# Performance work log

Measured on AMD Instinct MI355X. Metric: run time of the kernel, lower is better.

Reference implementation:

```python
import jax, jax.numpy as jnp
import numpy as np

N = 262144
BN_EPS = 1e-5


def gcn_conv(x, edge_index, edge_weight, W, b):
    """PyG GCNConv: symmetric norm with added self-loops (fill value 1).
    out[i] = sum_e d^{-1/2}[src] * w_e * d^{-1/2}[dst] * (x[src] @ W) + b
    """
    src, dst = edge_index[0], edge_index[1]
    loops = jnp.arange(N)
    src2 = jnp.concatenate([src, loops])
    dst2 = jnp.concatenate([dst, loops])
    ew2 = jnp.concatenate([edge_weight, jnp.ones((N,), edge_weight.dtype)])
    deg = jax.ops.segment_sum(ew2, dst2, num_segments=N)  # [N]
    dinv = jnp.where(deg > 0, jax.lax.rsqrt(deg), 0.0)
    norm = dinv[src2] * ew2 * dinv[dst2]  # [E+N]
    h = x @ W  # [N, out_c] tiny GEMM
    msg = h[src2] * norm[:, None]  # gather + scale, [E+N, out_c]
    out = jax.ops.segment_sum(msg, dst2, num_segments=N)  # scatter-add
    return out + b


def bn_eval(x, gamma, beta, mean, var):
    # BatchNorm1d in eval mode (running statistics)
    return (x - mean) * (gamma * jax.lax.rsqrt(var + BN_EPS)) + beta


def setup_inputs() -> dict:
    key = jax.random.key(0)
    ks = jax.random.split(key, 16)
    E = 4194304
    inp = {
        "x": jax.random.normal(ks[0], (N, 1), jnp.float32),
        "edge_index": jax.random.randint(ks[1], (2, E), 0, N, jnp.int64),
        "edge_weight": jax.random.uniform(ks[2], (E,), jnp.float32),
        # GCNConv weights (lin has no bias fused; bias added after aggregation)
        "W1": jax.random.normal(ks[3], (1, 16), jnp.float32) * 0.5,
        "b1": jnp.zeros((16,), jnp.float32),
        "W2": jax.random.normal(ks[4], (16, 4), jnp.float32) * 0.25,
        "b2": jnp.zeros((4,), jnp.float32),
        "W3": jax.random.normal(ks[5], (4, 1), jnp.float32) * 0.5,
        "b3": jnp.zeros((1,), jnp.float32),
        # BatchNorm params (eval-mode running stats)
        "g1": jnp.ones((16,), jnp.float32), "be1": jnp.zeros((16,), jnp.float32),
        "m1": jax.random.normal(ks[6], (16,), jnp.float32) * 0.1,
        "v1": jax.random.uniform(ks[7], (16,), jnp.float32, 0.5, 1.5),
        "g2": jnp.ones((4,), jnp.float32), "be2": jnp.zeros((4,), jnp.float32),
        "m2": jax.random.normal(ks[8], (4,), jnp.float32) * 0.1,
        "v2": jax.random.uniform(ks[9], (4,), jnp.float32, 0.5, 1.5),
        # final Linear
        "We": jax.random.normal(ks[10], (1, 1), jnp.float32),
        "bee": jnp.zeros((1,), jnp.float32),
    }
    return inp


def reference(x, edge_index, edge_weight, W1, b1, W2, b2, W3, b3,
              g1, be1, m1, v1, g2, be2, m2, v2, We, bee):
    h = gcn_conv(x, edge_index, edge_weight, W1, b1)
    h = jax.nn.relu(bn_eval(h, g1, be1, m1, v1))  # dropout = identity (eval)
    h = gcn_conv(h, edge_index, edge_weight, W2, b2)
    h = jax.nn.relu(bn_eval(h, g2, be2, m2, v2))
    h = gcn_conv(h, edge_index, edge_weight, W3, b3)
    h = h @ We + bee
    return jax.nn.sigmoid(h)
```

## Files before the change

kernel.cpp:

```cpp
#include <hip/hip_runtime.h>
#include <hip/hip_fp16.h>
#include <math.h>


#define BN_EPS 1e-5f
#define BKT_BITS 9
#define BKT_SZ 512
#define NBKT 512
#define PB 1024
#define PT 512
#define STAGE_CAP 4096
#define CAPR 8960
#define CHUNK_R 9
#define NGRP 128
#define NBL 2048
#define CAP2 2560
#define SW(p) ((p) ^ (((p) >> 5) & 31))

typedef int v2i __attribute__((ext_vector_type(2)));
typedef int v4i __attribute__((ext_vector_type(4)));

__device__ inline int2 ntload2(const int2* p) {
    v2i v = __builtin_nontemporal_load((const v2i*)p);
    return make_int2(v.x, v.y);
}
__device__ inline int4 ntload4(const int4* p) {
    v4i v = __builtin_nontemporal_load((const v4i*)p);
    return make_int4(v.x, v.y, v.z, v.w);
}
__device__ inline int ntloadi(const int* p) { return __builtin_nontemporal_load(p); }
__device__ inline void ntstore2(int2* p, int2 v) {
    v2i t; t.x = v.x; t.y = v.y;
    __builtin_nontemporal_store(t, (v2i*)p);
}
__device__ inline float wdec(int e) {
    return __half2float(__ushort_as_half((unsigned short)((((unsigned)e) >> 18) << 1)));
}

__global__ void k_zero(int* __restrict__ gcur, int m) {
    int i = blockIdx.x * blockDim.x + threadIdx.x;
    if (i < m) gcur[i] = 0;
}

__device__ inline void scat1(int d, int s, int wbits, int* __restrict__ cur,
                             const int* __restrict__ basem, int2* __restrict__ stage) {
    int bk = ((unsigned)d) >> BKT_BITS;
    int dloc = d & (BKT_SZ - 1);
    int pos = atomicAdd(&cur[bk], 1);
    int dest = basem[bk] + pos;
    unsigned h = (unsigned)(__half_as_ushort(__float2half(__int_as_float(wbits))) & 0x7FFF);
    unsigned w14 = (h >> 1) + (h & 1);
    stage[pos] = make_int2(
        (int)((unsigned)s | ((unsigned)dloc << 18) | (((unsigned)dest & 31u) << 27)),
        (int)(w14 | (((unsigned)dest >> 5) << 14)));
}

__global__ __launch_bounds__(PT, 8) void k_scatter(
        const int* __restrict__ src, const int* __restrict__ dst,
        const float* __restrict__ w, int* __restrict__ gcur,
        int2* __restrict__ sorted, int E) {
    __shared__ int cur[NBKT];
    __shared__ int basem[NBKT];
    __shared__ int wsum[8];
    __shared__ int2 stage[STAGE_CAP];
    int t = threadIdx.x, b = blockIdx.x;
    cur[t] = 0;
    __syncthreads();
    int lo = b * STAGE_CAP;
    const int4* dp = (const int4*)(dst + lo);
    const int4* sp = (const int4*)(src + lo);
    const int4* wp = (const int4*)(w + lo);
    int4 d4a = ntload4(dp + t);
    int4 d4b = ntload4(dp + t + PT);
    int4 s4a = ntload4(sp + t), s4b = ntload4(sp + t + PT);
    int4 w4a = ntload4(wp + t), w4b = ntload4(wp + t + PT);
    atomicAdd(&cur[((unsigned)d4a.x) >> BKT_BITS], 1);
    atomicAdd(&cur[((unsigned)d4a.y) >> BKT_BITS], 1);
    atomicAdd(&cur[((unsigned)d4a.z) >> BKT_BITS], 1);
    atomicAdd(&cur[((unsigned)d4a.w) >> BKT_BITS], 1);
    atomicAdd(&cur[((unsigned)d4b.x) >> BKT_BITS], 1);
    atomicAdd(&cur[((unsigned)d4b.y) >> BKT_BITS], 1);
    atomicAdd(&cur[((unsigned)d4b.z) >> BKT_BITS], 1);
    atomicAdd(&cur[((unsigned)d4b.w) >> BKT_BITS], 1);
    __syncthreads();
    int v = cur[t];
    int lane = t & 63, wid = t >> 6;
    int inc = v;
#pragma unroll
    for (int off = 1; off < 64; off <<= 1) {
        int u = __shfl_up(inc, off);
        if (lane >= off) inc += u;
    }
    if (lane == 63) wsum[wid] = inc;
    __syncthreads();
    if (t == 0) {
        int s = 0;
#pragma unroll
        for (int i = 0; i < 8; ++i) { int c = wsum[i]; wsum[i] = s; s += c; }
    }
    __syncthreads();
    int excl = inc - v + wsum[wid];
    int gbase = v ? atomicAdd(&gcur[t << 4], v) : 0;
    cur[t] = excl;
    basem[t] = t * CAPR + gbase - excl;
    __syncthreads();
    scat1(d4a.x, s4a.x, w4a.x, cur, basem, stage);
    scat1(d4a.y, s4a.y, w4a.y, cur, basem, stage);
    scat1(d4a.z, s4a.z, w4a.z, cur, basem, stage);
    scat1(d4a.w, s4a.w, w4a.w, cur, basem, stage);
    scat1(d4b.x, s4b.x, w4b.x, cur, basem, stage);
    scat1(d4b.y, s4b.y, w4b.y, cur, basem, stage);
    scat1(d4b.z, s4b.z, w4b.z, cur, basem, stage);
    scat1(d4b.w, s4b.w, w4b.w, cur, basem, stage);
    __syncthreads();
    for (int p = t; p < STAGE_CAP; p += PT) {
        int2 sv = stage[p];
        unsigned w0 = (unsigned)sv.x, w1 = (unsigned)sv.y;
        int dest = (int)(((w1 >> 14) << 5) | (w0 >> 27));
        ntstore2(&sorted[dest], make_int2((int)(w0 & 0x07FFFFFF), (int)(w1 & 0x3FFF)));
    }
}

__global__ __launch_bounds__(1024, 8) void k_sortdeg(
        const int* __restrict__ gcur, int2* __restrict__ sorted,
        const float* __restrict__ x, float* __restrict__ dinv,
        float* __restrict__ xs, int* __restrict__ starts,
        int* __restrict__ gend) {
    __shared__ int lpk[CAPR];
    __shared__ int cnt[BKT_SZ];
    __shared__ int sts[BKT_SZ + 1];
    __shared__ int wsum2[8];
    int t = threadIdx.x, b = blockIdx.x;
    int lo2 = b * CAPR;
    int len = min(gcur[b << 4], CAPR);
    if (t < BKT_SZ) cnt[t] = 0;
    __syncthreads();

    int e27[CHUNK_R], wrk[CHUNK_R];
#pragma unroll
    for (int r = 0; r < CHUNK_R; ++r) {
        int k = t + (r << 10);
        if (k < len) {
            int2 v = ntload2(&sorted[lo2 + k]);
            e27[r] = v.x;
            int rk = atomicAdd(&cnt[((unsigned)v.x) >> 18], 1);
            wrk[r] = (v.y & 0x3FFF) | (rk << 14);
        }
    }
    __syncthreads();
    int c_own = (t < BKT_SZ) ? cnt[t] : 0;
    int lane = t & 63, wid = t >> 6;
    int inc = c_own;
#pragma unroll
    for (int o = 1; o < 64; o <<= 1) {
        int u = __shfl_up(inc, o);
        if (lane >= o) inc += u;
    }
    if (t < BKT_SZ && lane == 63) wsum2[wid] = inc;
    __syncthreads();
    if (t == 0) {
        int s = 0;
#pragma unroll
        for (int i = 0; i < 8; ++i) { int c = wsum2[i]; wsum2[i] = s; s += c; }
    }
    __syncthreads();
    if (t < BKT_SZ) sts[t] = inc - c_own + wsum2[wid];
    if (t == 0) sts[BKT_SZ] = len;
    __syncthreads();
#pragma unroll
    for (int r = 0; r < CHUNK_R; ++r) {
        int k = t + (r << 10);
        if (k < len) {
            int e = e27[r];
            int pos = sts[((unsigned)e) >> 18] + (((unsigned)wrk[r]) >> 14);
            lpk[SW(pos)] = (e & 0x3FFFF) | ((wrk[r] & 0x3FFF) << 18);
        }
    }
    __syncthreads();

    int pbase = 2 * lo2;
    if (t < BKT_SZ) {
        int c0 = sts[t], c1 = sts[t + 1];
        float s = 0.f;
        for (int k = c0; k < c1; ++k) s += wdec(lpk[SW(k)]);
        float di = rsqrtf(1.0f + s);
        int i = b * BKT_SZ + t;
        dinv[i] = di;
        xs[i] = di * x[i];
        starts[i] = pbase + c0;
    }
    if (t < 4)
        gend[b * 4 + t] = pbase + ((t == 3) ? len : sts[(t + 1) * NGRP]);

    int* srtp = (int*)sorted;
    for (int k = t; k < len; k += 1024)
        srtp[pbase + k] = lpk[SW(k)];
}

__global__ __launch_bounds__(512, 8) void k_l1(
        const int* __restrict__ starts, const int* __restrict__ gend,
        const int* __restrict__ srtp,
        const float* __restrict__ xs, const float* __restrict__ dinv,
        const float* __restrict__ W1, const float* __restrict__ b1,
        const float* __restrict__ g1, const float* __restrict__ be1,
        const float* __restrict__ m1, const float* __restrict__ v1,
        const float* __restrict__ W2, int2* __restrict__ hs2p) {
    __shared__ int eds[CAP2];
    __shared__ float part[3][NGRP];
    int t = threadIdx.x, b = blockIdx.x;
    int i0 = b * NGRP;
    int lo = starts[i0];
    int len = min(gend[b] - lo, CAP2);
    for (int k = t; k < len; k += 512) eds[SW(k)] = ntloadi(srtp + lo + k);
    __syncthreads();
    int li = t & (NGRP - 1);
    int j = t >> 7;
    int i = i0 + li;
    int c0 = starts[i] - lo;
    int c1 = (li == NGRP - 1) ? len : starts[i + 1] - lo;
    int seg = c1 - c0;
    int kb = c0 + ((seg * j) >> 2);
    int ke = c0 + ((seg * (j + 1)) >> 2);
    float acc = 0.f;
    for (int k = kb; k < ke; ++k) {
        int e = eds[SW(k)];
        acc = fmaf(wdec(e), xs[e & 0x3FFFF], acc);
    }
    if (j) part[j - 1][li] = acc;
    __syncthreads();
    if (j) return;
    float di = dinv[i];
    float a = di * (acc + part[0][li] + part[1][li] + part[2][li] + xs[i]);
    float h0 = 0.f, h1 = 0.f, h2 = 0.f, h3 = 0.f;
#pragma unroll
    for (int c = 0; c < 16; ++c) {
        float s1c = g1[c] * rsqrtf(v1[c] + BN_EPS);
        float z = fmaf(a, W1[c] * s1c, fmaf(b1[c] - m1[c], s1c, be1[c]));
        z = fmaxf(z, 0.f);
        h0 = fmaf(z, W2[c * 4 + 0], h0);
        h1 = fmaf(z, W2[c * 4 + 1], h1);
        h2 = fmaf(z, W2[c * 4 + 2], h2);
        h3 = fmaf(z, W2[c * 4 + 3], h3);
    }
    __half2 p01 = __floats2half2_rn(di * h0, di * h1);
    __half2 p23 = __floats2half2_rn(di * h2, di * h3);
    hs2p[i] = make_int2(*(int*)&p01, *(int*)&p23);
}

__global__ __launch_bounds__(512, 8) void k_l2(
        const int* __restrict__ starts, const int* __restrict__ gend,
        const int* __restrict__ srtp,
        const int2* __restrict__ hs2p, const float* __restrict__ dinv,
        const float* __restrict__ b2, const float* __restrict__ g2,
        const float* __restrict__ be2, const float* __restrict__ m2,
        const float* __restrict__ v2, const float* __restrict__ W3,
        float* __restrict__ hs3) {
    __shared__ int eds[CAP2];
    __shared__ float4 part4[3][NGRP];
    int t = threadIdx.x, b = blockIdx.x;
    int i0 = b * NGRP;
    int lo = starts[i0];
    int len = min(gend[b] - lo, CAP2);
    for (int k = t; k < len; k += 512) eds[SW(k)] = ntloadi(srtp + lo + k);
    __syncthreads();
    int li = t & (NGRP - 1);
    int j = t >> 7;
    int i = i0 + li;
    int c0 = starts[i] - lo;
    int c1 = (li == NGRP - 1) ? len : starts[i + 1] - lo;
    int seg = c1 - c0;
    int kb = c0 + ((seg * j) >> 2);
    int ke = c0 + ((seg * (j + 1)) >> 2);
    float a0 = 0.f, a1 = 0.f, a2 = 0.f, a3 = 0.f;
    for (int k = kb; k < ke; ++k) {
        int e = eds[SW(k)];
        int2 h = hs2p[e & 0x3FFFF];
        float wv = wdec(e);
        float2 f01 = __half22float2(*(__half2*)&h.x);
        float2 f23 = __half22float2(*(__half2*)&h.y);
        a0 = fmaf(wv, f01.x, a0); a1 = fmaf(wv, f01.y, a1);
        a2 = fmaf(wv, f23.x, a2); a3 = fmaf(wv, f23.y, a3);
    }
    if (j) part4[j - 1][li] = make_float4(a0, a1, a2, a3);
    __syncthreads();
    if (j) return;
    float4 pa = part4[0][li], pb = part4[1][li], pc = part4[2][li];
    float di = dinv[i];
    int2 sp = hs2p[i];
    float2 f01 = __half22float2(*(__half2*)&sp.x);
    float2 f23 = __half22float2(*(__half2*)&sp.y);
    float av[4] = {di * (a0 + pa.x + pb.x + pc.x + f01.x),
                   di * (a1 + pa.y + pb.y + pc.y + f01.y),
                   di * (a2 + pa.z + pb.z + pc.z + f23.x),
                   di * (a3 + pa.w + pb.w + pc.w + f23.y)};
    float h = 0.f;
#pragma unroll
    for (int d = 0; d < 4; ++d) {
        float s2 = g2[d] * rsqrtf(v2[d] + BN_EPS);
        float z = fmaf(av[d] + b2[d] - m2[d], s2, be2[d]);
        z = fmaxf(z, 0.f);
        h = fmaf(z, W3[d], h);
    }
    hs3[i] = di * h;
}

__global__ __launch_bounds__(512, 8) void k_l3(
        const int* __restrict__ starts, const int* __restrict__ gend,
        const int* __restrict__ srtp,
        const float* __restrict__ hs3, const float* __restrict__ dinv,
        const float* __restrict__ b3, const float* __restrict__ We,
        const float* __restrict__ bee, float* __restrict__ out) {
    __shared__ int eds[CAP2];
    __shared__ float part[3][NGRP];
    int t = threadIdx.x, b = blockIdx.x;
    int i0 = b * NGRP;
    int lo = starts[i0];
    int len = min(gend[b] - lo, CAP2);
    for (int k = t; k < len; k += 512) eds[SW(k)] = ntloadi(srtp + lo + k);
    __syncthreads();
    int li = t & (NGRP - 1);
    int j = t >> 7;
    int i = i0 + li;
    int c0 = starts[i] - lo;
    int c1 = (li == NGRP - 1) ? len : starts[i + 1] - lo;
    int seg = c1 - c0;
    int kb = c0 + ((seg * j) >> 2);
    int ke = c0 + ((seg * (j + 1)) >> 2);
    float acc = 0.f;
    for (int k = kb; k < ke; ++k) {
        int e = eds[SW(k)];
        acc = fmaf(wdec(e), hs3[e & 0x3FFFF], acc);
    }
    if (j) part[j - 1][li] = acc;
    __syncthreads();
    if (j) return;
    float a = dinv[i] * (acc + part[0][li] + part[1][li] + part[2][li] + hs3[i]);
    float o = fmaf(a + b3[0], We[0], bee[0]);
    out[i] = 1.0f / (1.0f + expf(-o));
}

extern "C" void kernel_launch(void* const* d_in, const int* in_sizes, int n_in,
                              void* d_out, int out_size, void* d_ws, size_t ws_size,
                              hipStream_t stream) {
    const float* x   = (const float*)d_in[0];
    const int*   ei  = (const int*)d_in[1];
    const float* w   = (const float*)d_in[2];
    const float* W1  = (const float*)d_in[3];
    const float* b1  = (const float*)d_in[4];
    const float* W2  = (const float*)d_in[5];
    const float* b2  = (const float*)d_in[6];
    const float* W3  = (const float*)d_in[7];
    const float* b3  = (const float*)d_in[8];
    const float* g1  = (const float*)d_in[9];
    const float* be1 = (const float*)d_in[10];
    const float* m1  = (const float*)d_in[11];
    const float* v1  = (const float*)d_in[12];
    const float* g2  = (const float*)d_in[13];
    const float* be2 = (const float*)d_in[14];
    const float* m2  = (const float*)d_in[15];
    const float* v2  = (const float*)d_in[16];
    const float* We  = (const float*)d_in[17];
    const float* bee = (const float*)d_in[18];
    float* out = (float*)d_out;

    const int n = in_sizes[0];
    const int E = in_sizes[2];
    const int* src = ei;
    const int* dst = ei + E;

    char* ws = (char*)d_ws;
    int2*  sorted  = (int2*)ws;
    int*   gcur    = (int*)(ws + (size_t)NBKT * CAPR * 8);
    int2*  hs2p    = (int2*)(gcur + NBKT * 16);
    float* dinv    = (float*)(hs2p + n);
    float* xs      = dinv + n;
    float* hs3     = xs + n;
    int*   starts  = (int*)(hs3 + n);
    int*   gend    = starts + n;

    int* srtp = (int*)sorted;

    k_zero<<<(NBKT * 16 + 255) / 256, 256, 0, stream>>>(gcur, NBKT * 16);
    k_scatter<<<PB, PT, 0, stream>>>(src, dst, w, gcur, sorted, E);
    k_sortdeg<<<NBKT, 1024, 0, stream>>>(gcur, sorted, x, dinv, xs, starts, gend);
    k_l1<<<NBL, 512, 0, stream>>>(starts, gend, srtp, xs, dinv,
                                  W1, b1, g1, be1, m1, v1, W2, hs2p);
    k_l2<<<NBL, 512, 0, stream>>>(starts, gend, srtp, hs2p, dinv,
                                  b2, g2, be2, m2, v2, W3, hs3);
    k_l3<<<NBL, 512, 0, stream>>>(starts, gend, srtp, hs3, dinv, b3, We, bee, out);
}
```

Before: 252.4 us.

## Shard global bucket counters to cut atomic contention, software-pipeline gather loops

Each destination bucket's global cursor is split into 8 shards picked by block index, so scatter blocks contend on different atomics. Each shard writes into its own sub-region of the bucket. The sort kernel then reassembles the shards using prefix offsets, which adds a per-element shard lookup. Separately, the three aggregation loops are software-pipelined so the next gather load is issued before the current FMA, giving more memory-level parallelism. Per-shard capacity limits add a risk of truncation if a shard overflows.

```diff
diff --git a/kernel.cpp b/kernel.cpp
--- a/kernel.cpp
+++ b/kernel.cpp
@@ -10,7 +10,10 @@
 #define PB 1024
 #define PT 512
 #define STAGE_CAP 4096
-#define CAPR 8960
+#define SHD 8
+#define CAPS 1280
+#define CAPR (SHD*CAPS)
+#define CAPL 8960
 #define CHUNK_R 9
 #define NGRP 128
 #define NBL 2048
@@ -100,9 +103,10 @@
     }
     __syncthreads();
     int excl = inc - v + wsum[wid];
-    int gbase = v ? atomicAdd(&gcur[t << 4], v) : 0;
+    int shard = b & (SHD - 1);
+    int gbase = v ? atomicAdd(&gcur[((t << 3) | shard) << 4], v) : 0;
     cur[t] = excl;
-    basem[t] = t * CAPR + gbase - excl;
+    basem[t] = t * CAPR + shard * CAPS + gbase - excl;
     __syncthreads();
     scat1(d4a.x, s4a.x, w4a.x, cur, basem, stage);
     scat1(d4a.y, s4a.y, w4a.y, cur, basem, stage);
@@ -126,22 +130,35 @@
         const float* __restrict__ x, float* __restrict__ dinv,
         float* __restrict__ xs, int* __restrict__ starts,
         int* __restrict__ gend) {
-    __shared__ int lpk[CAPR];
+    __shared__ int lpk[CAPL];
     __shared__ int cnt[BKT_SZ];
     __shared__ int sts[BKT_SZ + 1];
     __shared__ int wsum2[8];
+    __shared__ int ssh[SHD];
+    __shared__ int soff[SHD + 1];
     int t = threadIdx.x, b = blockIdx.x;
-    int lo2 = b * CAPR;
-    int len = min(gcur[b << 4], CAPR);
     if (t < BKT_SZ) cnt[t] = 0;
-    __syncthreads();
+    if (t < SHD) ssh[t] = min(gcur[((b << 3) | t) << 4], CAPS);
+    __syncthreads();
+    if (t == 0) {
+        int s = 0;
+#pragma unroll
+        for (int i = 0; i < SHD; ++i) { soff[i] = s; s += ssh[i]; }
+        soff[SHD] = min(s, CAPL);
+    }
+    __syncthreads();
+    int len = soff[SHD];
+    int rbase = b * CAPR;
 
     int e27[CHUNK_R], wrk[CHUNK_R];
 #pragma unroll
     for (int r = 0; r < CHUNK_R; ++r) {
         int k = t + (r << 10);
         if (k < len) {
-            int2 v = ntload2(&sorted[lo2 + k]);
+            int s = 0;
+#pragma unroll
+            for (int q = 1; q < SHD; ++q) s += (k >= soff[q]) ? 1 : 0;
+            int2 v = ntload2(&sorted[rbase + s * CAPS + (k - soff[s])]);
             e27[r] = v.x;
             int rk = atomicAdd(&cnt[((unsigned)v.x) >> 18], 1);
             wrk[r] = (v.y & 0x3FFF) | (rk << 14);
@@ -178,7 +195,7 @@
     }
     __syncthreads();
 
-    int pbase = 2 * lo2;
+    int pbase = 2 * rbase;
     if (t < BKT_SZ) {
         int c0 = sts[t], c1 = sts[t + 1];
         float s = 0.f;
@@ -222,9 +239,17 @@
     int kb = c0 + ((seg * j) >> 2);
     int ke = c0 + ((seg * (j + 1)) >> 2);
     float acc = 0.f;
-    for (int k = kb; k < ke; ++k) {
+    int k = kb;
+    if (k < ke) {
         int e = eds[SW(k)];
-        acc = fmaf(wdec(e), xs[e & 0x3FFFF], acc);
+        float xv = xs[e & 0x3FFFF];
+        for (++k; k < ke; ++k) {
+            int e2 = eds[SW(k)];
+            float x2 = xs[e2 & 0x3FFFF];
+            acc = fmaf(wdec(e), xv, acc);
+            e = e2; xv = x2;
+        }
+        acc = fmaf(wdec(e), xv, acc);
     }
     if (j) part[j - 1][li] = acc;
     __syncthreads();
@@ -272,9 +297,20 @@
     int kb = c0 + ((seg * j) >> 2);
     int ke = c0 + ((seg * (j + 1)) >> 2);
     float a0 = 0.f, a1 = 0.f, a2 = 0.f, a3 = 0.f;
-    for (int k = kb; k < ke; ++k) {
+    int k = kb;
+    if (k < ke) {
         int e = eds[SW(k)];
         int2 h = hs2p[e & 0x3FFFF];
+        for (++k; k < ke; ++k) {
+            int e2 = eds[SW(k)];
+            int2 h2 = hs2p[e2 & 0x3FFFF];
+            float wv = wdec(e);
+            float2 f01 = __half22float2(*(__half2*)&h.x);
+            float2 f23 = __half22float2(*(__half2*)&h.y);
+            a0 = fmaf(wv, f01.x, a0); a1 = fmaf(wv, f01.y, a1);
+            a2 = fmaf(wv, f23.x, a2); a3 = fmaf(wv, f23.y, a3);
+            e = e2; h = h2;
+        }
         float wv = wdec(e);
         float2 f01 = __half22float2(*(__half2*)&h.x);
         float2 f23 = __half22float2(*(__half2*)&h.y);
@@ -327,9 +363,17 @@
     int kb = c0 + ((seg * j) >> 2);
     int ke = c0 + ((seg * (j + 1)) >> 2);
     float acc = 0.f;
-    for (int k = kb; k < ke; ++k) {
+    int k = kb;
+    if (k < ke) {
         int e = eds[SW(k)];
-        acc = fmaf(wdec(e), hs3[e & 0x3FFFF], acc);
+        float xv = hs3[e & 0x3FFFF];
+        for (++k; k < ke; ++k) {
+            int e2 = eds[SW(k)];
+            float x2 = hs3[e2 & 0x3FFFF];
+            acc = fmaf(wdec(e), xv, acc);
+            e = e2; xv = x2;
+        }
+        acc = fmaf(wdec(e), xv, acc);
     }
     if (j) part[j - 1][li] = acc;
     __syncthreads();
@@ -371,7 +415,7 @@
     char* ws = (char*)d_ws;
     int2*  sorted  = (int2*)ws;
     int*   gcur    = (int*)(ws + (size_t)NBKT * CAPR * 8);
-    int2*  hs2p    = (int2*)(gcur + NBKT * 16);
+    int2*  hs2p    = (int2*)(gcur + NBKT * SHD * 16);
     float* dinv    = (float*)(hs2p + n);
     float* xs      = dinv + n;
     float* hs3     = xs + n;
@@ -380,7 +424,7 @@
 
     int* srtp = (int*)sorted;
 
-    k_zero<<<(NBKT * 16 + 255) / 256, 256, 0, stream>>>(gcur, NBKT * 16);
+    k_zero<<<(NBKT * SHD * 16 + 255) / 256, 256, 0, stream>>>(gcur, NBKT * SHD * 16);
     k_scatter<<<PB, PT, 0, stream>>>(src, dst, w, gcur, sorted, E);
     k_sortdeg<<<NBKT, 1024, 0, stream>>>(gcur, sorted, x, dinv, xs, starts, gend);
     k_l1<<<NBL, 512, 0, stream>>>(starts, gend, srtp, xs, dinv,
```

New measurement: 247.3 us. -2.0%, faster.
